# Optimization experiments

Measured on AMD Instinct MI355X. Metric: run time of the kernel, lower is better.

## Reference

```python
import jax, jax.numpy as jnp
import numpy as np

N_NODES = 100000
N_EDGES = 3200000
DIM = 16


def setup_inputs() -> dict:
    key = jax.random.key(0)
    k1, k2, k3, k4 = jax.random.split(key, 4)
    state_input = jax.random.normal(k1, (N_NODES, DIM), dtype=jnp.float32)
    row = jax.random.randint(k2, (N_EDGES,), 0, N_NODES, dtype=jnp.int32)
    col = jax.random.randint(k3, (N_EDGES,), 0, N_NODES, dtype=jnp.int32)
    edge_weights = jax.random.uniform(k4, (N_EDGES,), dtype=jnp.float32)
    return {"state_input": state_input, "row": row, "col": col,
            "edge_weights": edge_weights}


def reference(state_input, row, col, edge_weights):
    # f_eq: per-dim self dynamics, f(x) = -x  -> [N, dim]
    self_diff = -state_input

    # gather pair endpoints: x_1 = state[col], x_2 = state[row]
    # g_eq: sin(x_2 - x_1) per dim (Kuramoto-style coupling) -> [E, dim]
    neighbor_processed = jnp.sin(state_input[row] - state_input[col])

    # weight by edge weight and scatter-sum into destination nodes (col)
    aggregated_sum = jax.ops.segment_sum(
        neighbor_processed * edge_weights[:, None], col,
        num_segments=state_input.shape[0])  # [N, dim]

    # s_eq: elementwise tanh on aggregated sum
    interact_diff = jnp.tanh(aggregated_sum)

    return (self_diff + interact_diff,
            (state_input, self_diff),
            (aggregated_sum, interact_diff))
```

## Files before the change

kernel.cpp:

```cpp
#include <hip/hip_runtime.h>
#include <hip/hip_fp16.h>
#include <math.h>

#define N_NODES 100000
#define N_EDGES 3200000
#define DIM 16
#define NSZ (N_NODES * DIM)

#define NPB 128
#define NBUCK 782
#define NBLK 512
#define EPB 6256
#define MAXCAP 5120
#define CAP 4864
#define PRK 5

typedef float nvec4 __attribute__((ext_vector_type(4)));

__device__ inline unsigned pack32(int c, int r, float ww) {
    unsigned w8 = (unsigned)fminf(ww * 256.0f, 255.0f);
    return ((unsigned)(c & 127) << 25) | ((unsigned)r << 8) | w8;
}

__global__ __launch_bounds__(1024)
void sort_write(const float* __restrict__ state, __half* __restrict__ hs,
                float* __restrict__ out,
                const int* __restrict__ row, const int* __restrict__ col,
                const float* __restrict__ w, int* __restrict__ cnt,
                unsigned* __restrict__ packed) {
    __shared__ int cur[NBUCK];
    int t = threadIdx.x, blk = blockIdx.x;
    int e0 = blk * EPB;
    int eN = e0 + EPB; if (eN > N_EDGES) eN = N_EDGES;
    int nch = (eN - e0) >> 2;
    const int4*   c4p = (const int4*)(col + e0);
    const int4*   r4p = (const int4*)(row + e0);
    const float4* w4p = (const float4*)(w + e0);

    for (int j = t; j < NBUCK; j += 1024) cur[j] = 0;

    {
        int i = blk * 1024 + t;
        if (i < NSZ / 4) {
            nvec4 v = __builtin_nontemporal_load(&((const nvec4*)state)[i]);
            union { __half2 h[2]; float2 f; } u;
            u.h[0] = __floats2half2_rn(v.x, v.y);
            u.h[1] = __floats2half2_rn(v.z, v.w);
            ((float2*)hs)[i] = u.f;
            __builtin_nontemporal_store(v, &((nvec4*)(out + 1 * (size_t)NSZ))[i]);
            nvec4 nv = {-v.x, -v.y, -v.z, -v.w};
            __builtin_nontemporal_store(nv, &((nvec4*)(out + 2 * (size_t)NSZ))[i]);
        }
    }
    __syncthreads();

    unsigned pr[8];
    int bb[8];
    #pragma unroll
    for (int k = 0; k < 2; ++k) {
        int i = t + k * 1024;
        if (i < nch) {
            int4 c = c4p[i]; int4 r = r4p[i]; float4 ww = w4p[i];
            pr[4 * k + 0] = pack32(c.x, r.x, ww.x); bb[4 * k + 0] = c.x >> 7;
            pr[4 * k + 1] = pack32(c.y, r.y, ww.y); bb[4 * k + 1] = c.y >> 7;
            pr[4 * k + 2] = pack32(c.z, r.z, ww.z); bb[4 * k + 2] = c.z >> 7;
            pr[4 * k + 3] = pack32(c.w, r.w, ww.w); bb[4 * k + 3] = c.w >> 7;
            atomicAdd(&cur[bb[4 * k + 0]], 1);
            atomicAdd(&cur[bb[4 * k + 1]], 1);
            atomicAdd(&cur[bb[4 * k + 2]], 1);
            atomicAdd(&cur[bb[4 * k + 3]], 1);
        }
    }
    __syncthreads();

    for (int j = t; j < NBUCK; j += 1024) {
        int v = cur[j];
        if (v) cur[j] = j * MAXCAP + atomicAdd(&cnt[j], v);
    }
    __syncthreads();

    #pragma unroll
    for (int k = 0; k < 2; ++k) {
        int i = t + k * 1024;
        if (i < nch) {
            #pragma unroll
            for (int j = 0; j < 4; ++j) {
                int pos = atomicAdd(&cur[bb[4 * k + j]], 1);
                packed[pos] = pr[4 * k + j];
            }
        }
    }
}

__global__ __launch_bounds__(1024, 8)
void aggregate(const float* __restrict__ state, const __half2* __restrict__ hs2,
               const int* __restrict__ cnt,
               const unsigned* __restrict__ packed,
               float* __restrict__ out) {
    __shared__ unsigned sbuf[CAP];
    __shared__ int s_cnt[NPB], s_start[NPB], s_cur[NPB];
    __shared__ int s_wsum;
    int nb = blockIdx.x, t = threadIdx.x;
    int q = t & 3, sub = (t >> 2) & 1, g = t >> 3;
    int beg = nb * MAXCAP;
    int end = beg + cnt[nb];
    int n = nb * NPB + g;
    bool valid = (n < N_NODES);
    float4 xx = valid ? ((const float4*)state)[n * 4 + q]
                      : make_float4(0.f, 0.f, 0.f, 0.f);
    float4 acc = {0.f, 0.f, 0.f, 0.f};
    const uint2* hsu = (const uint2*)hs2;

    for (int tbeg = beg; tbeg < end; tbeg += CAP) {
        int tend = tbeg + CAP; if (tend > end) tend = end;
        if (t < NPB) s_cnt[t] = 0;
        __syncthreads();

        unsigned pr[PRK];
        #pragma unroll
        for (int k = 0; k < PRK; ++k) {
            int e = tbeg + t + k * 1024;
            if (e < tend) {
                pr[k] = __builtin_nontemporal_load(&packed[e]);
                atomicAdd(&s_cnt[pr[k] >> 25], 1);
            }
        }
        __syncthreads();

        {
            int v = 0, ps = 0;
            if (t < NPB) {
                v = s_cnt[t]; ps = v;
                #pragma unroll
                for (int d = 1; d < 64; d <<= 1) {
                    int u = __shfl_up(ps, d, 64);
                    if ((t & 63) >= d) ps += u;
                }
            }
            if (t == 63) s_wsum = ps;
            __syncthreads();
            if (t < NPB) {
                int ex = ps - v + ((t >= 64) ? s_wsum : 0);
                s_start[t] = ex;
                s_cur[t] = ex;
            }
        }
        __syncthreads();

        #pragma unroll
        for (int k = 0; k < PRK; ++k) {
            int e = tbeg + t + k * 1024;
            if (e < tend) {
                int pos = atomicAdd(&s_cur[pr[k] >> 25], 1);
                sbuf[pos] = pr[k];
            }
        }
        __syncthreads();

        {
            int es = s_start[g], ee = s_cur[g];
            int e = es + sub;
            for (; e + 14 < ee; e += 16) {
                unsigned p0 = sbuf[e];
                unsigned p1 = sbuf[e + 2];
                unsigned p2 = sbuf[e + 4];
                unsigned p3 = sbuf[e + 6];
                unsigned p4 = sbuf[e + 8];
                unsigned p5 = sbuf[e + 10];
                unsigned p6 = sbuf[e + 12];
                unsigned p7 = sbuf[e + 14];
                uint2 h0 = hsu[((p0 >> 8) & 0x1FFFFu) * 4u + q];
                uint2 h1 = hsu[((p1 >> 8) & 0x1FFFFu) * 4u + q];
                uint2 h2 = hsu[((p2 >> 8) & 0x1FFFFu) * 4u + q];
                uint2 h3 = hsu[((p3 >> 8) & 0x1FFFFu) * 4u + q];
                uint2 h4 = hsu[((p4 >> 8) & 0x1FFFFu) * 4u + q];
                uint2 h5 = hsu[((p5 >> 8) & 0x1FFFFu) * 4u + q];
                uint2 h6 = hsu[((p6 >> 8) & 0x1FFFFu) * 4u + q];
                uint2 h7 = hsu[((p7 >> 8) & 0x1FFFFu) * 4u + q];
                #pragma unroll
                for (int j = 0; j < 8; ++j) {
                    unsigned p = (j == 0) ? p0 : (j == 1) ? p1 : (j == 2) ? p2
                               : (j == 3) ? p3 : (j == 4) ? p4 : (j == 5) ? p5
                               : (j == 6) ? p6 : p7;
                    uint2 hb = (j == 0) ? h0 : (j == 1) ? h1 : (j == 2) ? h2
                             : (j == 3) ? h3 : (j == 4) ? h4 : (j == 5) ? h5
                             : (j == 6) ? h6 : h7;
                    float we = ((float)(p & 255u) + 0.5f) * 0.00390625f;
                    float2 lo = __half22float2(*(const __half2*)&hb.x);
                    float2 hi = __half22float2(*(const __half2*)&hb.y);
                    acc.x += __sinf(lo.x - xx.x) * we;
                    acc.y += __sinf(lo.y - xx.y) * we;
                    acc.z += __sinf(hi.x - xx.z) * we;
                    acc.w += __sinf(hi.y - xx.w) * we;
                }
            }
            for (; e < ee; e += 2) {
                unsigned p = sbuf[e];
                uint2 hb = hsu[((p >> 8) & 0x1FFFFu) * 4u + q];
                float we = ((float)(p & 255u) + 0.5f) * 0.00390625f;
                float2 lo = __half22float2(*(const __half2*)&hb.x);
                float2 hi = __half22float2(*(const __half2*)&hb.y);
                acc.x += __sinf(lo.x - xx.x) * we;
                acc.y += __sinf(lo.y - xx.y) * we;
                acc.z += __sinf(hi.x - xx.z) * we;
                acc.w += __sinf(hi.y - xx.w) * we;
            }
        }
        __syncthreads();
    }

    acc.x += __shfl_xor(acc.x, 4, 64); acc.y += __shfl_xor(acc.y, 4, 64);
    acc.z += __shfl_xor(acc.z, 4, 64); acc.w += __shfl_xor(acc.w, 4, 64);

    if (valid && sub == 0) {
        float4 th = make_float4(tanhf(acc.x), tanhf(acc.y),
                                tanhf(acc.z), tanhf(acc.w));
        int gdx = n * 4 + q;
        nvec4 v0 = {th.x - xx.x, th.y - xx.y, th.z - xx.z, th.w - xx.w};
        nvec4 v3 = {acc.x, acc.y, acc.z, acc.w};
        nvec4 v4 = {th.x, th.y, th.z, th.w};
        __builtin_nontemporal_store(v0, &((nvec4*)(out + 0 * (size_t)NSZ))[gdx]);
        __builtin_nontemporal_store(v3, &((nvec4*)(out + 3 * (size_t)NSZ))[gdx]);
        __builtin_nontemporal_store(v4, &((nvec4*)(out + 4 * (size_t)NSZ))[gdx]);
    }
}

__global__ __launch_bounds__(256)
void edge_kernel(const float* __restrict__ state, const int* __restrict__ row,
                 const int* __restrict__ col, const float* __restrict__ w,
                 float* __restrict__ agg) {
    int idx = blockIdx.x * blockDim.x + threadIdx.x;
    if (idx >= N_EDGES * 4) return;
    int e = idx >> 2, qq = idx & 3;
    int r = row[e], c = col[e];
    float we = w[e];
    const float4 xr = ((const float4*)state)[r * 4 + qq];
    const float4 xcv = ((const float4*)state)[c * 4 + qq];
    float* dst = agg + c * DIM + qq * 4;
    atomicAdd(dst + 0, sinf(xr.x - xcv.x) * we);
    atomicAdd(dst + 1, sinf(xr.y - xcv.y) * we);
    atomicAdd(dst + 2, sinf(xr.z - xcv.z) * we);
    atomicAdd(dst + 3, sinf(xr.w - xcv.w) * we);
}

__global__ __launch_bounds__(256)
void node_kernel(const float* __restrict__ state, const float* __restrict__ agg,
                 float* __restrict__ out) {
    int idx = blockIdx.x * blockDim.x + threadIdx.x;
    if (idx >= N_NODES * 4) return;
    float4 x = ((const float4*)state)[idx];
    float4 a = ((const float4*)agg)[idx];
    float4 tv = make_float4(tanhf(a.x), tanhf(a.y), tanhf(a.z), tanhf(a.w));
    ((float4*)(out + 0 * NSZ))[idx] = make_float4(tv.x - x.x, tv.y - x.y,
                                                  tv.z - x.z, tv.w - x.w);
    ((float4*)(out + 1 * NSZ))[idx] = x;
    ((float4*)(out + 2 * NSZ))[idx] = make_float4(-x.x, -x.y, -x.z, -x.w);
    ((float4*)(out + 4 * NSZ))[idx] = tv;
}

extern "C" void kernel_launch(void* const* d_in, const int* in_sizes, int n_in,
                              void* d_out, int out_size, void* d_ws, size_t ws_size,
                              hipStream_t stream) {
    const float* state = (const float*)d_in[0];
    const int*   row   = (const int*)d_in[1];
    const int*   col   = (const int*)d_in[2];
    const float* w     = (const float*)d_in[3];
    float* out = (float*)d_out;

    size_t packed_off = 0;
    size_t hs_off     = packed_off + (size_t)NBUCK * MAXCAP * 4;
    size_t cnt_off    = hs_off + (size_t)NSZ * 2;
    size_t needed     = cnt_off + (size_t)NBUCK * 4;

    if (ws_size >= needed) {
        unsigned* packed = (unsigned*)((char*)d_ws + packed_off);
        __half* hs = (__half*)((char*)d_ws + hs_off);
        int* cnt   = (int*)((char*)d_ws + cnt_off);

        (void)hipMemsetAsync(cnt, 0, (size_t)NBUCK * sizeof(int), stream);
        sort_write<<<NBLK, 1024, 0, stream>>>(state, hs, out, row, col, w,
                                              cnt, packed);
        aggregate<<<NBUCK, 1024, 0, stream>>>(
            state, (const __half2*)hs, cnt, packed, out);
    } else {
        float* agg = out + 3 * NSZ;
        (void)hipMemsetAsync(agg, 0, NSZ * sizeof(float), stream);
        edge_kernel<<<(N_EDGES * 4 + 255) / 256, 256, 0, stream>>>(
            state, row, col, w, agg);
        node_kernel<<<(N_NODES * 4 + 255) / 256, 256, 0, stream>>>(
            state, agg, out);
    }
}
```

Baseline: 148.9 us.

## Stage bucketed edges in shared memory and write them out coalesced

The sort kernel now computes an exclusive prefix scan of the per-bucket counts and scatters the packed edges into a shared-memory buffer in bucket order. Each thread then streams that buffer to global memory, using a per-bucket offset to place each edge at its reserved slot. This replaces random per-edge global scatter writes with mostly contiguous runs, aiming for better write coalescing. The cost is about 37KB of extra LDS, which may reduce occupancy, plus an extra block-wide sync and scan.

```diff
diff --git a/kernel.cpp b/kernel.cpp
--- a/kernel.cpp
+++ b/kernel.cpp
@@ -28,11 +28,16 @@
                 const int* __restrict__ row, const int* __restrict__ col,
                 const float* __restrict__ w, int* __restrict__ cnt,
                 unsigned* __restrict__ packed) {
+    __shared__ unsigned sbuf[EPB];
+    __shared__ unsigned short sbkt[EPB];
     __shared__ int cur[NBUCK];
+    __shared__ int diff[NBUCK];
+    __shared__ int wsum[16];
     int t = threadIdx.x, blk = blockIdx.x;
     int e0 = blk * EPB;
     int eN = e0 + EPB; if (eN > N_EDGES) eN = N_EDGES;
-    int nch = (eN - e0) >> 2;
+    int ecnt = eN - e0;
+    int nch = ecnt >> 2;
     const int4*   c4p = (const int4*)(col + e0);
     const int4*   r4p = (const int4*)(row + e0);
     const float4* w4p = (const float4*)(w + e0);
@@ -73,9 +78,31 @@
     }
     __syncthreads();
 
-    for (int j = t; j < NBUCK; j += 1024) {
-        int v = cur[j];
-        if (v) cur[j] = j * MAXCAP + atomicAdd(&cnt[j], v);
+    {
+        int i0 = 2 * t, i1 = 2 * t + 1;
+        int v0 = (i0 < NBUCK) ? cur[i0] : 0;
+        int v1 = (i1 < NBUCK) ? cur[i1] : 0;
+        int p = v0 + v1, ps = p;
+        #pragma unroll
+        for (int d = 1; d < 64; d <<= 1) {
+            int u = __shfl_up(ps, d, 64);
+            if ((t & 63) >= d) ps += u;
+        }
+        if ((t & 63) == 63) wsum[t >> 6] = ps;
+        __syncthreads();
+        int wid = t >> 6, wbase = 0;
+        #pragma unroll
+        for (int k = 0; k < 16; ++k) wbase += (k < wid) ? wsum[k] : 0;
+        int ex = wbase + ps - p;
+        if (i0 < NBUCK) {
+            if (v0) diff[i0] = i0 * MAXCAP + atomicAdd(&cnt[i0], v0) - ex;
+            cur[i0] = ex;
+        }
+        if (i1 < NBUCK) {
+            int ex1 = ex + v0;
+            if (v1) diff[i1] = i1 * MAXCAP + atomicAdd(&cnt[i1], v1) - ex1;
+            cur[i1] = ex1;
+        }
     }
     __syncthreads();
 
@@ -85,10 +112,18 @@
         if (i < nch) {
             #pragma unroll
             for (int j = 0; j < 4; ++j) {
-                int pos = atomicAdd(&cur[bb[4 * k + j]], 1);
-                packed[pos] = pr[4 * k + j];
-            }
-        }
+                int b = bb[4 * k + j];
+                int pos = atomicAdd(&cur[b], 1);
+                sbuf[pos] = pr[4 * k + j];
+                sbkt[pos] = (unsigned short)b;
+            }
+        }
+    }
+    __syncthreads();
+
+    for (int i = t; i < ecnt; i += 1024) {
+        int b = (int)sbkt[i];
+        __builtin_nontemporal_store(sbuf[i], &packed[diff[b] + i]);
     }
 }
 
```

After: 158.4 us. 1.06x slower.
